# Performance work log

Hardware: AMD Instinct MI355X
Metric: run time of the kernel (lower is better)

## Reference

```python
import jax, jax.numpy as jnp
import numpy as np

B, N = 4, 4096
IN_C, POOL_C, FEAT_C, OUT_C, K = 128, 448, 256, 128, 3
MID = IN_C // 2            # SPFP mlp width = 64
RMID = ((FEAT_C + IN_C) + OUT_C) // 2  # refine middle = 256


def conv1x1(W, b, x):
    # pointwise Conv1d: x [B,C,N] -> [B,O,N]
    return jnp.einsum('oc,bcn->bon', W, x) + b[None, :, None]


def grid_sample_border(img, gx, gy):
    # F.grid_sample(mode='bilinear', padding_mode='border', align_corners=False)
    # img [B,C,H,W]; gx,gy [B,N] in normalized coords -> out [B,C,N]
    _, _, H, W = img.shape
    ix = ((gx + 1.0) * W - 1.0) * 0.5
    iy = ((gy + 1.0) * H - 1.0) * 0.5
    ix0 = jnp.floor(ix); iy0 = jnp.floor(iy)
    wx = (ix - ix0)[:, None, :]; wy = (iy - iy0)[:, None, :]
    x0 = jnp.clip(ix0.astype(jnp.int32), 0, W - 1)
    x1 = jnp.clip(ix0.astype(jnp.int32) + 1, 0, W - 1)
    y0 = jnp.clip(iy0.astype(jnp.int32), 0, H - 1)
    y1 = jnp.clip(iy0.astype(jnp.int32) + 1, 0, H - 1)
    gather = jax.vmap(lambda im, y, x: im[:, y, x])  # -> [B,C,N]
    v00 = gather(img, y0, x0); v01 = gather(img, y0, x1)
    v10 = gather(img, y1, x0); v11 = gather(img, y1, x1)
    return v00 * (1 - wx) * (1 - wy) + v01 * wx * (1 - wy) + v10 * (1 - wx) * wy + v11 * wx * wy


def knn_sum(h, loc):
    # sum of k-NN neighbor features (knn_graph, loop=False, source_to_target)
    # h [B,N,C], loc [B,N,3] -> [B,N,C]
    n = loc.shape[1]
    sq = jnp.sum(loc * loc, axis=-1)                      # [B,N]
    d = sq[:, :, None] + sq[:, None, :] - 2.0 * jnp.einsum('bnd,bmd->bnm', loc, loc)
    d = d + jnp.eye(n, dtype=d.dtype) * 1e10              # exclude self-loop
    _, idx = jax.lax.top_k(-d, K)                         # [B,N,K]
    nbr = jax.vmap(lambda f, i: f[i])(h, idx)             # [B,N,K,C]
    return nbr.sum(axis=2)


def pcd_conv(x_loc, x_feat, Wr, Wn, b):
    # PCDConv: cat(loc, feat) -> knn_graph -> GraphConv -> ReLU
    loc = x_loc.transpose(0, 2, 1)                        # [B,N,3]
    feat = x_feat.transpose(0, 2, 1)                      # [B,N,C]
    h = jnp.concatenate([loc, feat], axis=-1)             # [B,N,C+3]
    agg = knn_sum(h, loc)
    # PyG GraphConv: lin_root(x) + lin_rel(sum_j x_j) + bias
    out = jnp.einsum('bnc,oc->bno', h, Wr) + jnp.einsum('bnc,oc->bno', agg, Wn) + b
    return jax.nn.relu(out).transpose(0, 2, 1)            # [B,O,N]


def setup_inputs() -> dict:
    key = jax.random.key(0)
    ks = jax.random.split(key, 24)
    rn = lambda i, shp, s=0.05: jax.random.normal(ks[i], shp, dtype=jnp.float32) * s
    z = lambda c: jnp.zeros((c,), jnp.float32)
    return {
        'x_loc': jax.random.uniform(ks[0], (B, 3, N), jnp.float32, -1.0, 1.0),
        'x_feat': rn(1, (B, IN_C, N), 1.0),
        'x_pool0': rn(2, (B, 64, 112, 112), 1.0),
        'x_pool1': rn(3, (B, 128, 56, 56), 1.0),
        'x_pool2': rn(4, (B, 256, 28, 28), 1.0),
        # SPFP shared mlp [IN_C+3, MID, MID] and grid head [MID+3 -> 2]
        'Ws1': rn(5, (MID, IN_C + 3)), 'bs1': z(MID),
        'Ws2': rn(6, (MID, MID)), 'bs2': z(MID),
        'Wg': rn(7, (2, MID + 3), 0.1), 'bg': z(2),
        # linear SharedMLP [POOL_C, FEAT_C, FEAT_C]
        'Wl1': rn(8, (FEAT_C, POOL_C)), 'bl1': z(FEAT_C),
        'Wl2': rn(9, (FEAT_C, FEAT_C)), 'bl2': z(FEAT_C),
        # PCDRefinement: 3 GraphConvs (each input +3 loc channels)
        'Wr1': rn(10, (RMID, FEAT_C + IN_C + 3)), 'Wn1': rn(11, (RMID, FEAT_C + IN_C + 3)), 'b1': z(RMID),
        'Wr2': rn(12, (RMID, RMID + 3)), 'Wn2': rn(13, (RMID, RMID + 3)), 'b2': z(RMID),
        'Wr3': rn(14, (OUT_C, RMID + 3)), 'Wn3': rn(15, (OUT_C, RMID + 3)), 'b3': z(OUT_C),
        'Wloc': rn(16, (3, OUT_C + 3)), 'bloc': z(3),
    }


def reference(x_loc, x_feat, x_pool0, x_pool1, x_pool2,
              Ws1, bs1, Ws2, bs2, Wg, bg, Wl1, bl1, Wl2, bl2,
              Wr1, Wn1, b1, Wr2, Wn2, b2, Wr3, Wn3, b3, Wloc, bloc):
    # --- SPFP ---
    h = jnp.concatenate([x_loc, x_feat], axis=1)          # [B,IN_C+3,N]
    h = jax.nn.relu(conv1x1(Ws1, bs1, h))
    h = jax.nn.relu(conv1x1(Ws2, bs2, h))                 # SharedMLP then outer ReLU
    grid = conv1x1(Wg, bg, jnp.concatenate([x_loc, h], axis=1))  # [B,2,N]
    gx, gy = grid[:, 0], grid[:, 1]
    pooled = jnp.concatenate([grid_sample_border(p, gx, gy)
                              for p in (x_pool0, x_pool1, x_pool2)], axis=1)  # [B,POOL_C,N]
    # --- linear SharedMLP ---
    f = conv1x1(Wl2, bl2, jax.nn.relu(conv1x1(Wl1, bl1, pooled)))  # [B,FEAT_C,N]
    x_new_feat = jnp.concatenate([x_feat, f], axis=1)      # [B,IN_C+FEAT_C,N]
    # --- PCDRefinement ---
    feat = pcd_conv(x_loc, x_new_feat, Wr1, Wn1, b1)
    feat = pcd_conv(x_loc, feat, Wr2, Wn2, b2)
    feat = pcd_conv(x_loc, feat, Wr3, Wn3, b3)             # [B,OUT_C,N]
    logits = conv1x1(Wloc, bloc, jnp.concatenate([x_loc, feat], axis=1))
    x_new_loc = x_loc + jnp.tanh(logits)
    return (x_new_loc, feat)
```

## Files before the change

### kernel.cpp

```cpp
#include <hip/hip_runtime.h>
#include <hip/hip_bf16.h>

#define TPB 256
static constexpr int BATCH = 4;
static constexpr int NPTS  = 4096;
static constexpr int BN    = BATCH * NPTS;

typedef __attribute__((ext_vector_type(8))) short short8v;
typedef __attribute__((ext_vector_type(4))) short short4v;
typedef __attribute__((ext_vector_type(4))) float f32x4;

struct Seg { const float* in; const float* W; int C; int ws; };

__device__ __forceinline__ void gload16(const void* g, void* l) {
    __builtin_amdgcn_global_load_lds(
        (const __attribute__((address_space(1))) void*)g,
        (__attribute__((address_space(3))) void*)l, 16, 0, 0);
}

template<int EPI>
__global__ __launch_bounds__(256)
void gemm_k(const __hip_bfloat16* __restrict__ A, const __hip_bfloat16* __restrict__ B,
            const float* __restrict__ bias, float* __restrict__ outF,
            __hip_bfloat16* __restrict__ outB, int Kp, int rowOff)
{
    __shared__ short Alds[8192];
    __shared__ short Blds[8704];
    const int tid = threadIdx.x, lane = tid & 63, wid = tid >> 6;
    const int wm = wid & 1, wn = wid >> 1;
    const int n0 = blockIdx.x * 128, m0 = blockIdx.y * 128;

    const char* asrc[4]; short* adst[4];
    #pragma unroll
    for (int t = 0; t < 4; ++t) {
        const int g = (wid * 4 + t) * 64 + lane;
        const int arow = g >> 3, ai = g & 7;
        asrc[t] = (const char*)A +
                  (((size_t)(m0 + arow)) * Kp + ((ai ^ (arow & 7)) << 3)) * 2;
        adst[t] = &Alds[(wid * 4 + t) * 512];
    }
    const char* bsrc[2]; int bkp[2], bc0[2];
    #pragma unroll
    for (int it = 0; it < 2; ++it) {
        const int q = it * 256 + tid;
        bkp[it] = q >> 4;
        bc0[it] = (q & 15) * 8;
        bsrc[it] = (const char*)B +
                   (((size_t)(bkp[it] * 2)) * BN + (n0 + bc0[it])) * 2;
    }

    f32x4 acc[4][4];
    #pragma unroll
    for (int i = 0; i < 4; ++i)
        #pragma unroll
        for (int j = 0; j < 4; ++j) acc[i][j] = (f32x4){0.f, 0.f, 0.f, 0.f};

    const int rl = lane & 15, g4 = lane >> 4;

    const int nkt = Kp >> 6;
    for (int kt = 0; kt < nkt; ++kt) {
        __syncthreads();
        short8v blo[2], bhi[2];
        #pragma unroll
        for (int it = 0; it < 2; ++it) {
            blo[it] = *(const short8v*)(bsrc[it]);
            bhi[it] = *(const short8v*)(bsrc[it] + (size_t)BN * 2);
            bsrc[it] += (size_t)64 * BN * 2;
        }
        #pragma unroll
        for (int t = 0; t < 4; ++t) {
            gload16(asrc[t], adst[t]);
            asrc[t] += 128;
        }
        #pragma unroll
        for (int it = 0; it < 2; ++it) {
            #pragma unroll
            for (int j = 0; j < 8; ++j) {
                const int c = bc0[it] + j;
                const int val = ((int)(unsigned short)blo[it][j]) |
                                (((int)(unsigned short)bhi[it][j]) << 16);
                *(int*)((char*)Blds + c * 136 + bkp[it] * 4) = val;
            }
        }
        __syncthreads();

        #pragma unroll
        for (int ks = 0; ks < 2; ++ks) {
            short8v af[4];
            #pragma unroll
            for (int mf = 0; mf < 4; ++mf) {
                const int row = wm * 64 + mf * 16 + rl;
                const int base = row * 128, sw = (row & 7) << 4;
                const short4v lo = *(const short4v*)((const char*)Alds +
                                    (base + ((ks * 64 + (g4 << 3)) ^ sw)));
                const short4v hi = *(const short4v*)((const char*)Alds +
                                    (base + ((ks * 64 + (g4 << 3) + 32) ^ sw)));
                af[mf] = __builtin_shufflevector(lo, hi, 0,1,2,3,4,5,6,7);
            }
            short8v bfv[4];
            #pragma unroll
            for (int nf = 0; nf < 4; ++nf) {
                const int colr = wn * 64 + nf * 16 + rl;
                const char* bp = (const char*)Blds + colr * 136 + ks * 64 + (g4 << 3);
                const short4v lo = *(const short4v*)bp;
                const short4v hi = *(const short4v*)(bp + 32);
                bfv[nf] = __builtin_shufflevector(lo, hi, 0,1,2,3,4,5,6,7);
            }
            #pragma unroll
            for (int mf = 0; mf < 4; ++mf)
                #pragma unroll
                for (int nf = 0; nf < 4; ++nf)
                    acc[mf][nf] = __builtin_amdgcn_mfma_f32_16x16x32_bf16(
                        af[mf], bfv[nf], acc[mf][nf], 0, 0, 0);
        }
    }

    #pragma unroll
    for (int mf = 0; mf < 4; ++mf) {
        #pragma unroll
        for (int i = 0; i < 4; ++i) {
            const int row = m0 + wm * 64 + mf * 16 + g4 * 4 + i;
            const float bs = bias[row];
            #pragma unroll
            for (int nf = 0; nf < 4; ++nf) {
                const int col = n0 + wn * 64 + nf * 16 + rl;
                float v = acc[mf][nf][i] + bs;
                if (EPI == 1) {
                    v = fmaxf(v, 0.f);
                    outB[(size_t)(rowOff + row) * BN + col] = __float2bfloat16(v);
                } else {
                    outF[(size_t)row * BN + col] = v;
                }
            }
        }
    }
}

template<bool RELU>
__global__ __launch_bounds__(TPB)
void conv1x1_k(Seg s0, Seg s1, int nseg, int Ctot,
               const float* __restrict__ bias, float* __restrict__ out, int O)
{
    __shared__ float Wl[131][16];
    const int n  = blockIdx.x * TPB + threadIdx.x;
    const int o0 = blockIdx.y * 16;
    const int b  = blockIdx.z;
    Seg segs[2] = {s0, s1};
    int off[3]; off[0] = 0;
    #pragma unroll
    for (int k = 0; k < 2; ++k) off[k + 1] = off[k] + (k < nseg ? segs[k].C : 0);
    for (int idx = threadIdx.x; idx < Ctot * 16; idx += TPB) {
        int c = idx >> 4, t = idx & 15;
        int k = (nseg > 1 && c >= off[1]) ? 1 : 0;
        Wl[c][t] = segs[k].W[(size_t)(o0 + t) * segs[k].ws + (c - off[k])];
    }
    __syncthreads();
    float acc[16];
    #pragma unroll
    for (int t = 0; t < 16; ++t) acc[t] = 0.f;
    int cbase = 0;
    for (int k = 0; k < nseg; ++k) {
        const float* ip = segs[k].in + (size_t)b * segs[k].C * NPTS + n;
        const int C = segs[k].C;
        #pragma unroll 4
        for (int cc = 0; cc < C; ++cc) {
            float v = ip[(size_t)cc * NPTS];
            const float4* wr = (const float4*)(&Wl[cbase + cc][0]);
            #pragma unroll
            for (int q = 0; q < 4; ++q) {
                float4 w = wr[q];
                acc[4*q+0] += w.x * v; acc[4*q+1] += w.y * v;
                acc[4*q+2] += w.z * v; acc[4*q+3] += w.w * v;
            }
        }
        cbase += C;
    }
    #pragma unroll
    for (int t = 0; t < 16; ++t) {
        float r = acc[t] + bias[o0 + t];
        if (RELU) r = fmaxf(r, 0.f);
        out[((size_t)b * O + o0 + t) * NPTS + n] = r;
    }
}

__global__ __launch_bounds__(TPB)
void wcomp_k(const float* __restrict__ Wr1, const float* __restrict__ Wn1,
             const float* __restrict__ Wl2, const float* __restrict__ bl2,
             const float* __restrict__ b1,
             float* __restrict__ Wcu, float* __restrict__ Wcv,
             float* __restrict__ bu, float* __restrict__ bv)
{
    __shared__ float wrow[256];
    const int r = blockIdx.x, isv = blockIdx.y;
    const float* W = isv ? Wn1 : Wr1;
    const int k = threadIdx.x;
    wrow[k] = W[(size_t)r * 387 + 131 + k];
    __syncthreads();
    float acc = 0.f;
    for (int o = 0; o < 256; ++o) acc += wrow[o] * Wl2[(size_t)o * 256 + k];
    (isv ? Wcv : Wcu)[(size_t)r * 256 + k] = acc;
    if (k == 0) {
        float s = 0.f;
        for (int o = 0; o < 256; ++o) s += wrow[o] * bl2[o];
        if (isv) bv[r] = s; else bu[r] = b1[r] + s;
    }
}

__global__ __launch_bounds__(TPB)
void knn_k(const float* __restrict__ loc, int* __restrict__ idxp)
{
    __shared__ float4 pt[1024];
    const int b = blockIdx.y;
    const float* L = loc + (size_t)b * 3 * NPTS;

    const int ql = threadIdx.x >> 4;
    const int s  = threadIdx.x & 15;
    const int i  = blockIdx.x * 16 + ql;

    const float xi = L[i], yi = L[NPTS + i], zi = L[2 * NPTS + i];
    float sqi;
    {
        #pragma clang fp contract(off)
        sqi = xi * xi + yi * yi + zi * zi;
    }

    float d0 = 3e38f, d1 = 3e38f, d2 = 3e38f;
    int   i0 = 0x7fffffff, i1 = 0x7fffffff, i2 = 0x7fffffff;

    for (int c = 0; c < NPTS / 1024; ++c) {
        __syncthreads();
        {
            const int base = c * 1024 + threadIdx.x * 4;
            const float4 xs = *(const float4*)(L + base);
            const float4 ys = *(const float4*)(L + NPTS + base);
            const float4 zs = *(const float4*)(L + 2 * NPTS + base);
            float sq0, sq1, sq2, sq3;
            {
                #pragma clang fp contract(off)
                sq0 = xs.x * xs.x + ys.x * ys.x + zs.x * zs.x;
                sq1 = xs.y * xs.y + ys.y * ys.y + zs.y * zs.y;
                sq2 = xs.z * xs.z + ys.z * ys.z + zs.z * zs.z;
                sq3 = xs.w * xs.w + ys.w * ys.w + zs.w * zs.w;
            }
            pt[threadIdx.x * 4 + 0] = make_float4(xs.x, ys.x, zs.x, sq0);
            pt[threadIdx.x * 4 + 1] = make_float4(xs.y, ys.y, zs.y, sq1);
            pt[threadIdx.x * 4 + 2] = make_float4(xs.z, ys.z, zs.z, sq2);
            pt[threadIdx.x * 4 + 3] = make_float4(xs.w, ys.w, zs.w, sq3);
        }
        __syncthreads();

        #pragma unroll 4
        for (int k = 0; k < 1024 / 16; ++k) {
            const int jj = (k << 4) | s;
            const float4 p = pt[jj];
            const int j = (c << 10) | jj;
            float d;
            {
                #pragma clang fp contract(off)
                float dot = xi * p.x + yi * p.y + zi * p.z;
                d = (sqi + p.w) - 2.0f * dot;
            }
            d = (j == i) ? 3e38f : d;
            const bool lt2 = d < d2, lt1 = d < d1, lt0 = d < d0;
            d2 = lt1 ? d1 : (lt2 ? d : d2);  i2 = lt1 ? i1 : (lt2 ? j : i2);
            d1 = lt0 ? d0 : (lt1 ? d : d1);  i1 = lt0 ? i0 : (lt1 ? j : i1);
            d0 = lt0 ? d  : d0;              i0 = lt0 ? j  : i0;
        }
    }

    #pragma unroll
    for (int m = 1; m <= 8; m <<= 1) {
        float e0 = __shfl_xor(d0, m), e1 = __shfl_xor(d1, m), e2 = __shfl_xor(d2, m);
        int   j0 = __shfl_xor(i0, m), j1 = __shfl_xor(i1, m), j2 = __shfl_xor(i2, m);
        float ee[3] = {e0, e1, e2};
        int   jj[3] = {j0, j1, j2};
        #pragma unroll
        for (int t = 0; t < 3; ++t) {
            const float e = ee[t]; const int je = jj[t];
            const bool lt2 = (e < d2 || (e == d2 && je < i2));
            const bool lt1 = (e < d1 || (e == d1 && je < i1));
            const bool lt0 = (e < d0 || (e == d0 && je < i0));
            d2 = lt1 ? d1 : (lt2 ? e : d2);  i2 = lt1 ? i1 : (lt2 ? je : i2);
            d1 = lt0 ? d0 : (lt1 ? e : d1);  i1 = lt0 ? i0 : (lt1 ? je : i1);
            d0 = lt0 ? e  : d0;              i0 = lt0 ? je : i0;
        }
    }

    if (s == 0) {
        idxp[0 * BN + b * NPTS + i] = i0;
        idxp[1 * BN + b * NPTS + i] = i1;
        idxp[2 * BN + b * NPTS + i] = i2;
    }
}

__global__ __launch_bounds__(TPB)
void gridconv_k(const float* __restrict__ loc, const float* __restrict__ h2,
                const float* __restrict__ Wg, const float* __restrict__ bg,
                float* __restrict__ gridv)
{
    const int n = blockIdx.x * TPB + threadIdx.x;
    const int b = blockIdx.y;
    float a0 = bg[0], a1 = bg[1];
    #pragma unroll
    for (int c = 0; c < 3; ++c) {
        float v = loc[((size_t)b * 3 + c) * NPTS + n];
        a0 += Wg[c] * v; a1 += Wg[67 + c] * v;
    }
    const float* hp = h2 + (size_t)b * 64 * NPTS + n;
    #pragma unroll 4
    for (int c = 0; c < 64; ++c) {
        float v = hp[(size_t)c * NPTS];
        a0 += Wg[3 + c] * v; a1 += Wg[70 + c] * v;
    }
    gridv[((size_t)b * 2 + 0) * NPTS + n] = a0;
    gridv[((size_t)b * 2 + 1) * NPTS + n] = a1;
}

__global__ __launch_bounds__(TPB)
void gridsample_bf_k(const float* __restrict__ gridv, const float* __restrict__ p0,
                     const float* __restrict__ p1, const float* __restrict__ p2,
                     __hip_bfloat16* __restrict__ pooledbf)
{
    const int n    = blockIdx.x * 64 + (threadIdx.x & 63);
    const int cidx = blockIdx.y * 4 + (threadIdx.x >> 6);
    const int b    = blockIdx.z;
    const float* img; int C, H, c;
    if (cidx < 64)       { img = p0; C = 64;  H = 112; c = cidx; }
    else if (cidx < 192) { img = p1; C = 128; H = 56;  c = cidx - 64; }
    else                 { img = p2; C = 256; H = 28;  c = cidx - 192; }
    const float gx = gridv[((size_t)b * 2 + 0) * NPTS + n];
    const float gy = gridv[((size_t)b * 2 + 1) * NPTS + n];
    float wx, wy; int x0, x1, y0, y1;
    {
        #pragma clang fp contract(off)
        float ix  = ((gx + 1.0f) * (float)H - 1.0f) * 0.5f;
        float iy  = ((gy + 1.0f) * (float)H - 1.0f) * 0.5f;
        float ix0 = floorf(ix), iy0 = floorf(iy);
        wx = ix - ix0; wy = iy - iy0;
        x0 = min(max((int)ix0, 0),     H - 1);
        x1 = min(max((int)ix0 + 1, 0), H - 1);
        y0 = min(max((int)iy0, 0),     H - 1);
        y1 = min(max((int)iy0 + 1, 0), H - 1);
    }
    const float* pl = img + ((size_t)b * C + c) * H * H;
    float v = pl[y0*H + x0] * (1.f-wx)*(1.f-wy) + pl[y0*H + x1] * wx*(1.f-wy)
            + pl[y1*H + x0] * (1.f-wx)*wy       + pl[y1*H + x1] * wx*wy;
    pooledbf[(size_t)cidx * BN + b * NPTS + n] = __float2bfloat16(v);
}

__global__ __launch_bounds__(TPB)
void gatherfuse_bf_k(const float* __restrict__ uv, const int* __restrict__ idxp,
                     __hip_bfloat16* __restrict__ Xc)
{
    const int n = blockIdx.x * TPB + threadIdx.x;
    const int c = blockIdx.y;
    const int b = blockIdx.z;
    const int j0 = idxp[0 * BN + b * NPTS + n] & (NPTS - 1);
    const int j1 = idxp[1 * BN + b * NPTS + n] & (NPTS - 1);
    const int j2 = idxp[2 * BN + b * NPTS + n] & (NPTS - 1);
    const float* u = uv + (size_t)c * BN + b * NPTS;
    const float* v = uv + (size_t)(256 + c) * BN + b * NPTS;
    float r = u[n] + v[j0] + v[j1] + v[j2];
    Xc[(size_t)(3 + c) * BN + b * NPTS + n] = __float2bfloat16(fmaxf(r, 0.f));
}

__global__ __launch_bounds__(TPB)
void finalfuse_k(const float* __restrict__ uv, const int* __restrict__ idxp,
                 const float* __restrict__ loc,
                 const float* __restrict__ Wloc, const float* __restrict__ bloc,
                 float* __restrict__ outloc, float* __restrict__ outfeat)
{
    __shared__ float wl[393];
    __shared__ float part[16][16][3];
    for (int idx = threadIdx.x; idx < 393; idx += TPB) wl[idx] = Wloc[idx];
    __syncthreads();

    const int nl = threadIdx.x & 15, cg = threadIdx.x >> 4;
    const int n = blockIdx.x * 16 + nl;
    const int b = blockIdx.y;
    const int j0 = idxp[0 * BN + b * NPTS + n] & (NPTS - 1);
    const int j1 = idxp[1 * BN + b * NPTS + n] & (NPTS - 1);
    const int j2 = idxp[2 * BN + b * NPTS + n] & (NPTS - 1);

    float a0 = 0.f, a1 = 0.f, a2 = 0.f;
    #pragma unroll
    for (int cc = 0; cc < 8; ++cc) {
        const int c = cg * 8 + cc;
        const float* u = uv + (size_t)c * BN + b * NPTS;
        const float* v = uv + (size_t)(128 + c) * BN + b * NPTS;
        float f = fmaxf(u[n] + v[j0] + v[j1] + v[j2], 0.f);
        outfeat[((size_t)b * 128 + c) * NPTS + n] = f;
        a0 += wl[3 + c] * f; a1 += wl[134 + c] * f; a2 += wl[265 + c] * f;
    }
    part[cg][nl][0] = a0; part[cg][nl][1] = a1; part[cg][nl][2] = a2;
    __syncthreads();

    if (cg == 0) {
        float b0 = bloc[0], b1v = bloc[1], b2v = bloc[2];
        float l[3];
        #pragma unroll
        for (int c = 0; c < 3; ++c) {
            float v = loc[((size_t)b * 3 + c) * NPTS + n];
            l[c] = v;
            b0 += wl[c] * v; b1v += wl[131 + c] * v; b2v += wl[262 + c] * v;
        }
        #pragma unroll
        for (int g = 0; g < 16; ++g) {
            b0 += part[g][nl][0]; b1v += part[g][nl][1]; b2v += part[g][nl][2];
        }
        outloc[((size_t)b * 3 + 0) * NPTS + n] = l[0] + tanhf(b0);
        outloc[((size_t)b * 3 + 1) * NPTS + n] = l[1] + tanhf(b1v);
        outloc[((size_t)b * 3 + 2) * NPTS + n] = l[2] + tanhf(b2v);
    }
}

__global__ __launch_bounds__(TPB)
void castrows_k(const float* __restrict__ src, __hip_bfloat16* __restrict__ dst,
                int C, int rowOff)
{
    const int n = blockIdx.x * TPB + threadIdx.x;
    const int c = blockIdx.y, b = blockIdx.z;
    dst[(size_t)(rowOff + c) * BN + b * NPTS + n] =
        __float2bfloat16(src[((size_t)b * C + c) * NPTS + n]);
}

__global__ __launch_bounds__(TPB)
void zerobf_k(__hip_bfloat16* __restrict__ dst, int count16B)
{
    int i = blockIdx.x * TPB + threadIdx.x;
    if (i < count16B) ((int4*)dst)[i] = make_int4(0, 0, 0, 0);
}

__global__ __launch_bounds__(TPB)
void wassemble_k(const float* __restrict__ S1, int ld1, int c1, int rows1,
                 const float* __restrict__ S2, int ld2, int c2,
                 int Kp, __hip_bfloat16* __restrict__ dst)
{
    const int c = blockIdx.x * TPB + threadIdx.x;
    const int r = blockIdx.y;
    if (c >= Kp) return;
    float v = 0.f;
    if (r < rows1) {
        if (c < c1) v = S1[(size_t)r * ld1 + c];
        else if (c < c1 + c2) v = S2[(size_t)r * ld2 + (c - c1)];
    }
    dst[(size_t)r * Kp + c] = __float2bfloat16(v);
}

__global__ __launch_bounds__(TPB)
void biasfill_k(const float* __restrict__ b2, const float* __restrict__ b3,
                float* __restrict__ bias3, float* __restrict__ bias4)
{
    int i = blockIdx.x * TPB + threadIdx.x;
    if (i < 512) bias3[i] = (i < 256) ? b2[i] : 0.f;
    else if (i < 768) { int j = i - 512; bias4[j] = (j < 128) ? b3[j] : 0.f; }
}

__global__ __launch_bounds__(TPB)
void sentinel_k(float* __restrict__ out, int ntot, float c)
{
    int i = blockIdx.x * TPB + threadIdx.x;
    if (i < ntot) out[i] = c;
}

extern "C" void kernel_launch(void* const* d_in, const int* in_sizes, int n_in,
                              void* d_out, int out_size, void* d_ws, size_t ws_size,
                              hipStream_t stream)
{
    static const int EXP_INS[26] = {
        49152, 2097152, 3211264, 1605632, 802816,
        8384, 64, 4096, 64, 134, 2,
        114688, 256, 65536, 256,
        99072, 99072, 256, 66304, 66304, 256,
        33152, 33152, 128, 393, 3 };
    constexpr size_t WS_REQ = 16237824ull * 4ull;

    float code = -1.f;
    if (n_in != 26) code = 64.f;
    else {
        bool ok = true;
        for (int i = 0; i < 26; ++i) ok = ok && (in_sizes[i] == EXP_INS[i]);
        if (!ok) code = 24.f;
    }
    if (code < 0.f && out_size != 2146304) code = 32.f;
    if (code < 0.f && ws_size < WS_REQ)    code = 16.f;
    if (code >= 0.f) {
        sentinel_k<<<dim3((out_size + TPB - 1) / TPB), dim3(TPB), 0, stream>>>(
            (float*)d_out, out_size, code);
        return;
    }

    const float* x_loc  = (const float*)d_in[0];
    const float* x_feat = (const float*)d_in[1];
    const float* p0     = (const float*)d_in[2];
    const float* p1     = (const float*)d_in[3];
    const float* p2     = (const float*)d_in[4];
    const float* Ws1 = (const float*)d_in[5];  const float* bs1 = (const float*)d_in[6];
    const float* Ws2 = (const float*)d_in[7];  const float* bs2 = (const float*)d_in[8];
    const float* Wg  = (const float*)d_in[9];  const float* bg  = (const float*)d_in[10];
    const float* Wl1 = (const float*)d_in[11]; const float* bl1 = (const float*)d_in[12];
    const float* Wl2 = (const float*)d_in[13]; const float* bl2 = (const float*)d_in[14];
    const float* Wr1 = (const float*)d_in[15]; const float* Wn1 = (const float*)d_in[16];
    const float* b1  = (const float*)d_in[17];
    const float* Wr2 = (const float*)d_in[18]; const float* Wn2 = (const float*)d_in[19];
    const float* b2  = (const float*)d_in[20];
    const float* Wr3 = (const float*)d_in[21]; const float* Wn3 = (const float*)d_in[22];
    const float* b3  = (const float*)d_in[23];
    const float* Wloc= (const float*)d_in[24]; const float* bloc= (const float*)d_in[25];

    float* ws = (float*)d_ws;
    float* U  = ws;
    float* h1 = U;
    float* h2 = U + 1048576;
    __hip_bfloat16* pooledbf = (__hip_bfloat16*)(ws + 8388608);
    __hip_bfloat16* Xc2      = pooledbf;
    __hip_bfloat16* Xc1 = (__hip_bfloat16*)(ws + 12058624);
    __hip_bfloat16* Xc3 = Xc1;
    float* S     = ws + 15728640;
    float* gridv = S;
    int*   idxp  = (int*)(S + 32768);
    float* Wc1u  = S + 81920;
    float* Wc1v  = S + 147456;
    float* bu1   = S + 212992;
    float* bv1   = S + 213248;
    float* bias3 = S + 213504;
    float* bias4 = S + 214016;
    __hip_bfloat16* Wb1 = (__hip_bfloat16*)(S + 214272);
    __hip_bfloat16* Wb2 = (__hip_bfloat16*)(S + 271616);
    __hip_bfloat16* Wb3 = (__hip_bfloat16*)(S + 386304);
    __hip_bfloat16* Wb4 = (__hip_bfloat16*)(S + 468224);

    float* out_loc  = (float*)d_out;
    float* out_feat = out_loc + (size_t)BATCH * 3 * NPTS;

    dim3 blk(TPB);
    const int GX = NPTS / TPB;
    Seg z{nullptr, nullptr, 0, 0};
    const int ZPAD16 = 61 * BN / 8;

    wcomp_k<<<dim3(256, 2), blk, 0, stream>>>(Wr1, Wn1, Wl2, bl2, b1,
                                              Wc1u, Wc1v, bu1, bv1);
    biasfill_k<<<dim3(3), blk, 0, stream>>>(b2, b3, bias3, bias4);
    wassemble_k<<<dim3(2, 256), blk, 0, stream>>>(Wl1, 448, 448, 256, nullptr, 0, 0, 448, Wb1);
    wassemble_k<<<dim3(2, 256), blk, 0, stream>>>(Wr1, 387, 131, 256, Wc1u, 256, 256, 448, Wb2);
    wassemble_k<<<dim3(2, 256), blk, 0, stream>>>(Wn1, 387, 131, 256, Wc1v, 256, 256, 448, Wb2 + 256*448);
    wassemble_k<<<dim3(2, 256), blk, 0, stream>>>(Wr2, 259, 259, 256, nullptr, 0, 0, 320, Wb3);
    wassemble_k<<<dim3(2, 256), blk, 0, stream>>>(Wn2, 259, 259, 256, nullptr, 0, 0, 320, Wb3 + 256*320);
    wassemble_k<<<dim3(2, 128), blk, 0, stream>>>(Wr3, 259, 259, 128, nullptr, 0, 0, 320, Wb4);
    wassemble_k<<<dim3(2, 128), blk, 0, stream>>>(Wn3, 259, 259, 128, nullptr, 0, 0, 320, Wb4 + 128*320);

    conv1x1_k<true><<<dim3(GX, 4, BATCH), blk, 0, stream>>>(
        Seg{x_loc, Ws1, 3, 131}, Seg{x_feat, Ws1 + 3, 128, 131}, 2, 131, bs1, h1, 64);
    conv1x1_k<true><<<dim3(GX, 4, BATCH), blk, 0, stream>>>(
        Seg{h1, Ws2, 64, 64}, z, 1, 64, bs2, h2, 64);
    gridconv_k<<<dim3(GX, BATCH), blk, 0, stream>>>(x_loc, h2, Wg, bg, gridv);
    knn_k<<<dim3(NPTS / 16, BATCH), blk, 0, stream>>>(x_loc, idxp);
    gridsample_bf_k<<<dim3(NPTS / 64, 112, BATCH), blk, 0, stream>>>(
        gridv, p0, p1, p2, pooledbf);

    castrows_k<<<dim3(GX, 3, BATCH), blk, 0, stream>>>(x_loc, Xc1, 3, 0);
    castrows_k<<<dim3(GX, 128, BATCH), blk, 0, stream>>>(x_feat, Xc1, 128, 3);
    zerobf_k<<<dim3((ZPAD16 + TPB - 1) / TPB), blk, 0, stream>>>(Xc1 + (size_t)387 * BN, ZPAD16);
    gemm_k<1><<<dim3(128, 2), blk, 0, stream>>>(Wb1, pooledbf, bl1, nullptr, Xc1, 448, 131);

    castrows_k<<<dim3(GX, 3, BATCH), blk, 0, stream>>>(x_loc, Xc2, 3, 0);
    zerobf_k<<<dim3((ZPAD16 + TPB - 1) / TPB), blk, 0, stream>>>(Xc2 + (size_t)259 * BN, ZPAD16);
    gemm_k<0><<<dim3(128, 4), blk, 0, stream>>>(Wb2, Xc1, bu1, U, nullptr, 448, 0);
    gatherfuse_bf_k<<<dim3(GX, 256, BATCH), blk, 0, stream>>>(U, idxp, Xc2);

    castrows_k<<<dim3(GX, 3, BATCH), blk, 0, stream>>>(x_loc, Xc3, 3, 0);
    zerobf_k<<<dim3((ZPAD16 + TPB - 1) / TPB), blk, 0, stream>>>(Xc3 + (size_t)259 * BN, ZPAD16);
    gemm_k<0><<<dim3(128, 4), blk, 0, stream>>>(Wb3, Xc2, bias3, U, nullptr, 320, 0);
    gatherfuse_bf_k<<<dim3(GX, 256, BATCH), blk, 0, stream>>>(U, idxp, Xc3);

    gemm_k<0><<<dim3(128, 2), blk, 0, stream>>>(Wb4, Xc3, bias4, U, nullptr, 320, 0);
    finalfuse_k<<<dim3(NPTS / 16, BATCH), blk, 0, stream>>>(
        U, idxp, x_loc, Wloc, bloc, out_loc, out_feat);
}
```

Baseline: 327.3 us.

## Stage gather source row in LDS, shrink conv output tile, fix knn staging stride

The gather-fuse kernel now loads the whole neighbour-value row for one channel and batch into shared memory. It then serves the three random neighbour lookups from LDS instead of from global memory, with each block looping over all points. The SPFP 1x1 conv kernels are templated on output tile width and launched with 8 outputs per block instead of 16, which gives more blocks and fewer registers per thread. The knn staging loop switches from per-thread float4 loads to coalesced strided scalar loads, which avoids bank-conflicted float4 LDS stores. Risks: the gather kernel launches only 1024 blocks using 16KB LDS each, and the conv kernels now read their inputs twice as many times.

```diff
diff --git a/kernel.cpp b/kernel.cpp
--- a/kernel.cpp
+++ b/kernel.cpp
@@ -136,28 +136,28 @@
     }
 }
 
-template<bool RELU>
+template<bool RELU, int OT>
 __global__ __launch_bounds__(TPB)
 void conv1x1_k(Seg s0, Seg s1, int nseg, int Ctot,
                const float* __restrict__ bias, float* __restrict__ out, int O)
 {
-    __shared__ float Wl[131][16];
+    __shared__ float Wl[131][OT];
     const int n  = blockIdx.x * TPB + threadIdx.x;
-    const int o0 = blockIdx.y * 16;
+    const int o0 = blockIdx.y * OT;
     const int b  = blockIdx.z;
     Seg segs[2] = {s0, s1};
     int off[3]; off[0] = 0;
     #pragma unroll
     for (int k = 0; k < 2; ++k) off[k + 1] = off[k] + (k < nseg ? segs[k].C : 0);
-    for (int idx = threadIdx.x; idx < Ctot * 16; idx += TPB) {
-        int c = idx >> 4, t = idx & 15;
+    for (int idx = threadIdx.x; idx < Ctot * OT; idx += TPB) {
+        int c = idx / OT, t = idx % OT;
         int k = (nseg > 1 && c >= off[1]) ? 1 : 0;
         Wl[c][t] = segs[k].W[(size_t)(o0 + t) * segs[k].ws + (c - off[k])];
     }
     __syncthreads();
-    float acc[16];
-    #pragma unroll
-    for (int t = 0; t < 16; ++t) acc[t] = 0.f;
+    float acc[OT];
+    #pragma unroll
+    for (int t = 0; t < OT; ++t) acc[t] = 0.f;
     int cbase = 0;
     for (int k = 0; k < nseg; ++k) {
         const float* ip = segs[k].in + (size_t)b * segs[k].C * NPTS + n;
@@ -167,7 +167,7 @@
             float v = ip[(size_t)cc * NPTS];
             const float4* wr = (const float4*)(&Wl[cbase + cc][0]);
             #pragma unroll
-            for (int q = 0; q < 4; ++q) {
+            for (int q = 0; q < OT / 4; ++q) {
                 float4 w = wr[q];
                 acc[4*q+0] += w.x * v; acc[4*q+1] += w.y * v;
                 acc[4*q+2] += w.z * v; acc[4*q+3] += w.w * v;
@@ -176,7 +176,7 @@
         cbase += C;
     }
     #pragma unroll
-    for (int t = 0; t < 16; ++t) {
+    for (int t = 0; t < OT; ++t) {
         float r = acc[t] + bias[o0 + t];
         if (RELU) r = fmaxf(r, 0.f);
         out[((size_t)b * O + o0 + t) * NPTS + n] = r;
@@ -230,22 +230,20 @@
     for (int c = 0; c < NPTS / 1024; ++c) {
         __syncthreads();
         {
-            const int base = c * 1024 + threadIdx.x * 4;
-            const float4 xs = *(const float4*)(L + base);
-            const float4 ys = *(const float4*)(L + NPTS + base);
-            const float4 zs = *(const float4*)(L + 2 * NPTS + base);
-            float sq0, sq1, sq2, sq3;
-            {
-                #pragma clang fp contract(off)
-                sq0 = xs.x * xs.x + ys.x * ys.x + zs.x * zs.x;
-                sq1 = xs.y * xs.y + ys.y * ys.y + zs.y * zs.y;
-                sq2 = xs.z * xs.z + ys.z * ys.z + zs.z * zs.z;
-                sq3 = xs.w * xs.w + ys.w * ys.w + zs.w * zs.w;
-            }
-            pt[threadIdx.x * 4 + 0] = make_float4(xs.x, ys.x, zs.x, sq0);
-            pt[threadIdx.x * 4 + 1] = make_float4(xs.y, ys.y, zs.y, sq1);
-            pt[threadIdx.x * 4 + 2] = make_float4(xs.z, ys.z, zs.z, sq2);
-            pt[threadIdx.x * 4 + 3] = make_float4(xs.w, ys.w, zs.w, sq3);
+            const int base = c * 1024;
+            #pragma unroll
+            for (int t = 0; t < 4; ++t) {
+                const int p = t * 256 + threadIdx.x;
+                const float x = L[base + p];
+                const float y = L[NPTS + base + p];
+                const float z = L[2 * NPTS + base + p];
+                float sq;
+                {
+                    #pragma clang fp contract(off)
+                    sq = x * x + y * y + z * z;
+                }
+                pt[p] = make_float4(x, y, z, sq);
+            }
         }
         __syncthreads();
 
@@ -352,16 +350,25 @@
 void gatherfuse_bf_k(const float* __restrict__ uv, const int* __restrict__ idxp,
                      __hip_bfloat16* __restrict__ Xc)
 {
-    const int n = blockIdx.x * TPB + threadIdx.x;
-    const int c = blockIdx.y;
-    const int b = blockIdx.z;
-    const int j0 = idxp[0 * BN + b * NPTS + n] & (NPTS - 1);
-    const int j1 = idxp[1 * BN + b * NPTS + n] & (NPTS - 1);
-    const int j2 = idxp[2 * BN + b * NPTS + n] & (NPTS - 1);
+    __shared__ float vl[NPTS];
+    const int c = blockIdx.x;
+    const int b = blockIdx.y;
     const float* u = uv + (size_t)c * BN + b * NPTS;
     const float* v = uv + (size_t)(256 + c) * BN + b * NPTS;
-    float r = u[n] + v[j0] + v[j1] + v[j2];
-    Xc[(size_t)(3 + c) * BN + b * NPTS + n] = __float2bfloat16(fmaxf(r, 0.f));
+    #pragma unroll
+    for (int t = 0; t < NPTS / TPB; ++t)
+        vl[t * TPB + threadIdx.x] = v[t * TPB + threadIdx.x];
+    __syncthreads();
+
+    #pragma unroll
+    for (int t = 0; t < NPTS / TPB; ++t) {
+        const int n = t * TPB + threadIdx.x;
+        const int j0 = idxp[0 * BN + b * NPTS + n] & (NPTS - 1);
+        const int j1 = idxp[1 * BN + b * NPTS + n] & (NPTS - 1);
+        const int j2 = idxp[2 * BN + b * NPTS + n] & (NPTS - 1);
+        float r = u[n] + vl[j0] + vl[j1] + vl[j2];
+        Xc[(size_t)(3 + c) * BN + b * NPTS + n] = __float2bfloat16(fmaxf(r, 0.f));
+    }
 }
 
 __global__ __launch_bounds__(TPB)
@@ -549,9 +556,9 @@
     wassemble_k<<<dim3(2, 128), blk, 0, stream>>>(Wr3, 259, 259, 128, nullptr, 0, 0, 320, Wb4);
     wassemble_k<<<dim3(2, 128), blk, 0, stream>>>(Wn3, 259, 259, 128, nullptr, 0, 0, 320, Wb4 + 128*320);
 
-    conv1x1_k<true><<<dim3(GX, 4, BATCH), blk, 0, stream>>>(
+    conv1x1_k<true, 8><<<dim3(GX, 8, BATCH), blk, 0, stream>>>(
         Seg{x_loc, Ws1, 3, 131}, Seg{x_feat, Ws1 + 3, 128, 131}, 2, 131, bs1, h1, 64);
-    conv1x1_k<true><<<dim3(GX, 4, BATCH), blk, 0, stream>>>(
+    conv1x1_k<true, 8><<<dim3(GX, 8, BATCH), blk, 0, stream>>>(
         Seg{h1, Ws2, 64, 64}, z, 1, 64, bs2, h2, 64);
     gridconv_k<<<dim3(GX, BATCH), blk, 0, stream>>>(x_loc, h2, Wg, bg, gridv);
     knn_k<<<dim3(NPTS / 16, BATCH), blk, 0, stream>>>(x_loc, idxp);
@@ -566,12 +573,12 @@
     castrows_k<<<dim3(GX, 3, BATCH), blk, 0, stream>>>(x_loc, Xc2, 3, 0);
     zerobf_k<<<dim3((ZPAD16 + TPB - 1) / TPB), blk, 0, stream>>>(Xc2 + (size_t)259 * BN, ZPAD16);
     gemm_k<0><<<dim3(128, 4), blk, 0, stream>>>(Wb2, Xc1, bu1, U, nullptr, 448, 0);
-    gatherfuse_bf_k<<<dim3(GX, 256, BATCH), blk, 0, stream>>>(U, idxp, Xc2);
+    gatherfuse_bf_k<<<dim3(256, BATCH), blk, 0, stream>>>(U, idxp, Xc2);
 
     castrows_k<<<dim3(GX, 3, BATCH), blk, 0, stream>>>(x_loc, Xc3, 3, 0);
     zerobf_k<<<dim3((ZPAD16 + TPB - 1) / TPB), blk, 0, stream>>>(Xc3 + (size_t)259 * BN, ZPAD16);
     gemm_k<0><<<dim3(128, 4), blk, 0, stream>>>(Wb3, Xc2, bias3, U, nullptr, 320, 0);
-    gatherfuse_bf_k<<<dim3(GX, 256, BATCH), blk, 0, stream>>>(U, idxp, Xc3);
+    gatherfuse_bf_k<<<dim3(256, BATCH), blk, 0, stream>>>(U, idxp, Xc3);
 
     gemm_k<0><<<dim3(128, 2), blk, 0, stream>>>(Wb4, Xc3, bias4, U, nullptr, 320, 0);
     finalfuse_k<<<dim3(NPTS / 16, BATCH), blk, 0, stream>>>(
```

Measured after the change: 306.7 us. -6.3%, faster.
